# Kernel tuning notes

Hardware: AMD Instinct MI355X
Metric: run time of the kernel (lower is better)

Reference implementation:

```python
import jax, jax.numpy as jnp
import numpy as np

N = 131072   # octree nodes at this depth
C = 192      # channels (depthwise)
K = 27       # 3x3x3 neighbor stencil
BN_EPS = 1e-5


def setup_inputs() -> dict:
    key = jax.random.key(0)
    k1, k2, k3 = jax.random.split(key, 3)
    data = jax.random.normal(k1, (N, C), dtype=jnp.float32)
    # Octree neighbor table: for each node, indices of its 27 stencil neighbors.
    neigh = jax.random.randint(k2, (N, K), 0, N)
    # Depthwise weights [K, C] (OctreeDWConv, use_bias=False)
    weight = jax.random.normal(k3, (K, C), dtype=jnp.float32) * 0.05
    gamma = jnp.ones((C,), dtype=jnp.float32)
    beta = jnp.zeros((C,), dtype=jnp.float32)
    return {"data": data, "neigh": neigh, "weight": weight,
            "gamma": gamma, "beta": beta}


def reference(data, neigh, weight, gamma, beta):
    # Depthwise octree conv: out[n, c] = sum_k data[neigh[n, k], c] * weight[k, c]
    # Scan over the 27 stencil taps so we never materialize the [N, K, C] gather.
    def step(acc, kin):
        idx_k, w_k = kin          # idx_k: [N], w_k: [C]
        return acc + data[idx_k] * w_k, None

    acc0 = jnp.zeros_like(data)
    out, _ = jax.lax.scan(step, acc0, (neigh.T, weight))  # out: [N, C]

    # BatchNorm1d (training mode: batch statistics over the node dimension)
    mean = jnp.mean(out, axis=0)
    var = jnp.var(out, axis=0)
    return (out - mean) * jax.lax.rsqrt(var + BN_EPS) * gamma + beta
```

## Files before the change

### kernel.cpp

```cpp
#include <hip/hip_runtime.h>


static constexpr int NN = 131072;
static constexpr int CC = 192;
static constexpr int KK = 27;
static constexpr int NB = 32;
static constexpr float BN_EPS = 1e-5f;

__device__ __forceinline__ unsigned short f2bf_rne(float x) {
    unsigned u = __float_as_uint(x);
    return (unsigned short)((u + 0x7FFFu + ((u >> 16) & 1u)) >> 16);
}

__global__ __launch_bounds__(256) void cvt_zero(
    const float* __restrict__ src, unsigned short* __restrict__ dst,
    float* __restrict__ stats )
{
    if (blockIdx.x < 2 && threadIdx.x < CC)
        stats[blockIdx.x * CC + threadIdx.x] = 0.f;

    const int i = blockIdx.x * 256 + threadIdx.x;
    const float4 v = reinterpret_cast<const float4*>(src)[i];
    ushort4 o;
    o.x = f2bf_rne(v.x); o.y = f2bf_rne(v.y);
    o.z = f2bf_rne(v.z); o.w = f2bf_rne(v.w);
    reinterpret_cast<ushort4*>(dst)[i] = o;
}

__global__ __launch_bounds__(192, 8) void conv_r4(
    const unsigned short* __restrict__ data_bf,
    const int*   __restrict__ neigh,
    const float* __restrict__ weight,
    unsigned short* __restrict__ conv_bf,
    float*       __restrict__ ch_sum,
    float*       __restrict__ ch_sumsq)
{
    __shared__ float lds_w[KK * CC];

    const int c    = threadIdx.x;
    const int base = blockIdx.x * NB;

#pragma unroll
    for (int k = 0; k < KK; ++k) lds_w[k * CC + c] = weight[k * CC + c];
    __syncthreads();

    float s = 0.f, ss = 0.f;

    for (int n = 0; n < NB; ++n) {
        const int node = base + n;
        const int* nrow = neigh + node * KK;

        unsigned short r[KK];
#pragma unroll
        for (int k = 0; k < KK; ++k)
            r[k] = data_bf[(size_t)nrow[k] * CC + c];

        float acc = 0.f;
#pragma unroll
        for (int k = 0; k < KK; ++k)
            acc = fmaf(__uint_as_float((unsigned)r[k] << 16),
                       lds_w[k * CC + c], acc);

        conv_bf[(size_t)node * CC + c] = f2bf_rne(acc);
        s  += acc;
        ss += acc * acc;
    }

    atomicAdd(&ch_sum[c],   s);
    atomicAdd(&ch_sumsq[c], ss);
}

__global__ __launch_bounds__(192) void bn_apply_fused(
    const uint2* __restrict__ conv_bf,
    const float* __restrict__ ch_sum,
    const float* __restrict__ ch_sumsq,
    const float* __restrict__ gamma,
    const float* __restrict__ beta,
    float* __restrict__ out)
{
    const int t = threadIdx.x;
    const int g = t / 48;
    const int q = t - g * 48;
    const int cb = q * 4;

    const float inv_n = 1.0f / (float)NN;
    float4 sc, bi;
    {
        float m0 = ch_sum[cb + 0] * inv_n, m1 = ch_sum[cb + 1] * inv_n;
        float m2 = ch_sum[cb + 2] * inv_n, m3 = ch_sum[cb + 3] * inv_n;
        float v0 = ch_sumsq[cb + 0] * inv_n - m0 * m0;
        float v1 = ch_sumsq[cb + 1] * inv_n - m1 * m1;
        float v2 = ch_sumsq[cb + 2] * inv_n - m2 * m2;
        float v3 = ch_sumsq[cb + 3] * inv_n - m3 * m3;
        sc.x = gamma[cb + 0] * rsqrtf(v0 + BN_EPS);
        sc.y = gamma[cb + 1] * rsqrtf(v1 + BN_EPS);
        sc.z = gamma[cb + 2] * rsqrtf(v2 + BN_EPS);
        sc.w = gamma[cb + 3] * rsqrtf(v3 + BN_EPS);
        bi.x = beta[cb + 0] - m0 * sc.x;
        bi.y = beta[cb + 1] - m1 * sc.y;
        bi.z = beta[cb + 2] - m2 * sc.z;
        bi.w = beta[cb + 3] - m3 * sc.w;
    }

    for (int nb = blockIdx.x; nb < NN / 4; nb += gridDim.x) {
        const int node = nb * 4 + g;
        const int i = node * 48 + q;
        const uint2 u = conv_bf[i];
        float4 v;
        v.x = fmaf(__uint_as_float(u.x << 16),         sc.x, bi.x);
        v.y = fmaf(__uint_as_float(u.x & 0xFFFF0000u), sc.y, bi.y);
        v.z = fmaf(__uint_as_float(u.y << 16),         sc.z, bi.z);
        v.w = fmaf(__uint_as_float(u.y & 0xFFFF0000u), sc.w, bi.w);
        reinterpret_cast<float4*>(out)[i] = v;
    }
}

__global__ __launch_bounds__(CC) void conv_bn_partial_f32(
    const float* __restrict__ data,
    const int*   __restrict__ neigh,
    const float* __restrict__ weight,
    float*       __restrict__ conv_out,
    float*       __restrict__ ch_sum,
    float*       __restrict__ ch_sumsq)
{
    const int c = threadIdx.x;
    const int base = blockIdx.x * NB;
    if (blockIdx.x < 2 && c < CC) {  }
    float w[KK];
#pragma unroll
    for (int k = 0; k < KK; ++k) w[k] = weight[k * CC + c];
    float s = 0.f, ss = 0.f;
    for (int n = 0; n < NB; ++n) {
        const int node = base + n;
        const int* nrow = neigh + node * KK;
        float acc = 0.f;
#pragma unroll
        for (int k = 0; k < KK; ++k)
            acc = fmaf(data[nrow[k] * CC + c], w[k], acc);
        conv_out[node * CC + c] = acc;
        s += acc; ss += acc * acc;
    }
    atomicAdd(&ch_sum[c], s);
    atomicAdd(&ch_sumsq[c], ss);
}

__global__ __launch_bounds__(192) void bn_apply_f32_fused(
    float* __restrict__ out,
    const float* __restrict__ ch_sum,
    const float* __restrict__ ch_sumsq,
    const float* __restrict__ gamma,
    const float* __restrict__ beta)
{
    const int t = threadIdx.x;
    const int g = t / 48;
    const int q = t - g * 48;
    const int cb = q * 4;
    const float inv_n = 1.0f / (float)NN;
    float4 sc, bi;
    float m0 = ch_sum[cb+0]*inv_n, m1 = ch_sum[cb+1]*inv_n;
    float m2 = ch_sum[cb+2]*inv_n, m3 = ch_sum[cb+3]*inv_n;
    sc.x = gamma[cb+0]*rsqrtf(ch_sumsq[cb+0]*inv_n - m0*m0 + BN_EPS);
    sc.y = gamma[cb+1]*rsqrtf(ch_sumsq[cb+1]*inv_n - m1*m1 + BN_EPS);
    sc.z = gamma[cb+2]*rsqrtf(ch_sumsq[cb+2]*inv_n - m2*m2 + BN_EPS);
    sc.w = gamma[cb+3]*rsqrtf(ch_sumsq[cb+3]*inv_n - m3*m3 + BN_EPS);
    bi.x = beta[cb+0] - m0*sc.x; bi.y = beta[cb+1] - m1*sc.y;
    bi.z = beta[cb+2] - m2*sc.z; bi.w = beta[cb+3] - m3*sc.w;
    for (int nb = blockIdx.x; nb < NN / 4; nb += gridDim.x) {
        const int i = (nb * 4 + g) * 48 + q;
        float4 v = reinterpret_cast<float4*>(out)[i];
        v.x = fmaf(v.x, sc.x, bi.x); v.y = fmaf(v.y, sc.y, bi.y);
        v.z = fmaf(v.z, sc.z, bi.z); v.w = fmaf(v.w, sc.w, bi.w);
        reinterpret_cast<float4*>(out)[i] = v;
    }
}

extern "C" void kernel_launch(void* const* d_in, const int* in_sizes, int n_in,
                              void* d_out, int out_size, void* d_ws, size_t ws_size,
                              hipStream_t stream) {
    const float* data   = (const float*)d_in[0];
    const int*   neigh  = (const int*)  d_in[1];
    const float* weight = (const float*)d_in[2];
    const float* gamma  = (const float*)d_in[3];
    const float* beta   = (const float*)d_in[4];
    float* out = (float*)d_out;

    float* stats    = (float*)d_ws;
    float* ch_sum   = stats;
    float* ch_sumsq = stats + CC;
    unsigned short* data_bf = (unsigned short*)((char*)d_ws + 4096);
    const size_t stage_bytes = (size_t)NN * CC * sizeof(unsigned short);
    unsigned short* conv_bf =
        (unsigned short*)((char*)d_ws + 4096 + stage_bytes);

    const size_t need_full = 4096 + 2 * stage_bytes;
    const int vec_grid = (NN * CC / 4) / 256;

    if (ws_size >= need_full) {
        cvt_zero<<<vec_grid, 256, 0, stream>>>(data, data_bf, stats);
        conv_r4<<<NN / NB, 192, 0, stream>>>(
            data_bf, neigh, weight, conv_bf, ch_sum, ch_sumsq);
        bn_apply_fused<<<8192, 192, 0, stream>>>(
            (const uint2*)conv_bf, ch_sum, ch_sumsq, gamma, beta, out);
    } else {
        hipMemsetAsync(stats, 0, 2 * CC * sizeof(float), stream);
        conv_bn_partial_f32<<<NN / NB, CC, 0, stream>>>(
            data, neigh, weight, out, ch_sum, ch_sumsq);
        bn_apply_f32_fused<<<8192, 192, 0, stream>>>(
            out, ch_sum, ch_sumsq, gamma, beta);
    }
}
```

Measured before the change: 406.7 us.

## Fuse convert, conv and BN apply into one cooperative persistent kernel

Replaces the three launches (bf16 conversion with stats zeroing, gather conv with per-channel statistics, BN apply) with a single cooperative kernel. The grid is sized from the occupancy query, and the phases are separated by grid-wide syncs. The aim is to remove inter-kernel launch gaps and tail effects. In exchange it adds two grid barriers and a host occupancy query, and it turns the conv and apply phases into grid-stride loops over a smaller, persistent grid.

```diff
diff --git a/kernel.cpp b/kernel.cpp
--- a/kernel.cpp
+++ b/kernel.cpp
@@ -1,4 +1,7 @@
 #include <hip/hip_runtime.h>
+#include <hip/hip_cooperative_groups.h>
+
+namespace cg = cooperative_groups;
 
 
 static constexpr int NN = 131072;
@@ -12,106 +15,102 @@
     return (unsigned short)((u + 0x7FFFu + ((u >> 16) & 1u)) >> 16);
 }
 
-__global__ __launch_bounds__(256) void cvt_zero(
-    const float* __restrict__ src, unsigned short* __restrict__ dst,
-    float* __restrict__ stats )
-{
-    if (blockIdx.x < 2 && threadIdx.x < CC)
-        stats[blockIdx.x * CC + threadIdx.x] = 0.f;
-
-    const int i = blockIdx.x * 256 + threadIdx.x;
-    const float4 v = reinterpret_cast<const float4*>(src)[i];
-    ushort4 o;
-    o.x = f2bf_rne(v.x); o.y = f2bf_rne(v.y);
-    o.z = f2bf_rne(v.z); o.w = f2bf_rne(v.w);
-    reinterpret_cast<ushort4*>(dst)[i] = o;
-}
-
-__global__ __launch_bounds__(192, 8) void conv_r4(
-    const unsigned short* __restrict__ data_bf,
+__global__ __launch_bounds__(192, 8) void fused_all(
+    const float* __restrict__ data,
     const int*   __restrict__ neigh,
     const float* __restrict__ weight,
-    unsigned short* __restrict__ conv_bf,
-    float*       __restrict__ ch_sum,
-    float*       __restrict__ ch_sumsq)
-{
-    __shared__ float lds_w[KK * CC];
-
-    const int c    = threadIdx.x;
-    const int base = blockIdx.x * NB;
-
-#pragma unroll
-    for (int k = 0; k < KK; ++k) lds_w[k * CC + c] = weight[k * CC + c];
-    __syncthreads();
-
-    float s = 0.f, ss = 0.f;
-
-    for (int n = 0; n < NB; ++n) {
-        const int node = base + n;
-        const int* nrow = neigh + node * KK;
-
-        unsigned short r[KK];
-#pragma unroll
-        for (int k = 0; k < KK; ++k)
-            r[k] = data_bf[(size_t)nrow[k] * CC + c];
-
-        float acc = 0.f;
-#pragma unroll
-        for (int k = 0; k < KK; ++k)
-            acc = fmaf(__uint_as_float((unsigned)r[k] << 16),
-                       lds_w[k * CC + c], acc);
-
-        conv_bf[(size_t)node * CC + c] = f2bf_rne(acc);
-        s  += acc;
-        ss += acc * acc;
-    }
-
-    atomicAdd(&ch_sum[c],   s);
-    atomicAdd(&ch_sumsq[c], ss);
-}
-
-__global__ __launch_bounds__(192) void bn_apply_fused(
-    const uint2* __restrict__ conv_bf,
-    const float* __restrict__ ch_sum,
-    const float* __restrict__ ch_sumsq,
     const float* __restrict__ gamma,
     const float* __restrict__ beta,
+    unsigned short* __restrict__ data_bf,
+    unsigned short* __restrict__ conv_bf,
+    float* __restrict__ stats,
     float* __restrict__ out)
 {
+    cg::grid_group grid = cg::this_grid();
+    __shared__ float lds_w[KK * CC];
+
     const int t = threadIdx.x;
-    const int g = t / 48;
-    const int q = t - g * 48;
-    const int cb = q * 4;
-
-    const float inv_n = 1.0f / (float)NN;
-    float4 sc, bi;
+
+#pragma unroll
+    for (int k = 0; k < KK; ++k) lds_w[k * CC + t] = weight[k * CC + t];
+
+    if (blockIdx.x == 0) { stats[t] = 0.f; stats[CC + t] = 0.f; }
     {
-        float m0 = ch_sum[cb + 0] * inv_n, m1 = ch_sum[cb + 1] * inv_n;
-        float m2 = ch_sum[cb + 2] * inv_n, m3 = ch_sum[cb + 3] * inv_n;
-        float v0 = ch_sumsq[cb + 0] * inv_n - m0 * m0;
-        float v1 = ch_sumsq[cb + 1] * inv_n - m1 * m1;
-        float v2 = ch_sumsq[cb + 2] * inv_n - m2 * m2;
-        float v3 = ch_sumsq[cb + 3] * inv_n - m3 * m3;
-        sc.x = gamma[cb + 0] * rsqrtf(v0 + BN_EPS);
-        sc.y = gamma[cb + 1] * rsqrtf(v1 + BN_EPS);
-        sc.z = gamma[cb + 2] * rsqrtf(v2 + BN_EPS);
-        sc.w = gamma[cb + 3] * rsqrtf(v3 + BN_EPS);
-        bi.x = beta[cb + 0] - m0 * sc.x;
-        bi.y = beta[cb + 1] - m1 * sc.y;
-        bi.z = beta[cb + 2] - m2 * sc.z;
-        bi.w = beta[cb + 3] - m3 * sc.w;
-    }
-
-    for (int nb = blockIdx.x; nb < NN / 4; nb += gridDim.x) {
-        const int node = nb * 4 + g;
-        const int i = node * 48 + q;
-        const uint2 u = conv_bf[i];
-        float4 v;
-        v.x = fmaf(__uint_as_float(u.x << 16),         sc.x, bi.x);
-        v.y = fmaf(__uint_as_float(u.x & 0xFFFF0000u), sc.y, bi.y);
-        v.z = fmaf(__uint_as_float(u.y << 16),         sc.z, bi.z);
-        v.w = fmaf(__uint_as_float(u.y & 0xFFFF0000u), sc.w, bi.w);
-        reinterpret_cast<float4*>(out)[i] = v;
+        const int total4 = NN * CC / 4;
+        for (int i = blockIdx.x * 192 + t; i < total4; i += gridDim.x * 192) {
+            const float4 v = reinterpret_cast<const float4*>(data)[i];
+            ushort4 o;
+            o.x = f2bf_rne(v.x); o.y = f2bf_rne(v.y);
+            o.z = f2bf_rne(v.z); o.w = f2bf_rne(v.w);
+            reinterpret_cast<ushort4*>(data_bf)[i] = o;
+        }
+    }
+    grid.sync();
+
+    {
+        float s = 0.f, ss = 0.f;
+        for (int chunk = blockIdx.x; chunk < NN / NB; chunk += gridDim.x) {
+            const int base = chunk * NB;
+            for (int n = 0; n < NB; ++n) {
+                const int node = base + n;
+                const int* nrow = neigh + node * KK;
+
+                unsigned short r[KK];
+#pragma unroll
+                for (int k = 0; k < KK; ++k)
+                    r[k] = data_bf[(size_t)nrow[k] * CC + t];
+
+                float acc = 0.f;
+#pragma unroll
+                for (int k = 0; k < KK; ++k)
+                    acc = fmaf(__uint_as_float((unsigned)r[k] << 16),
+                               lds_w[k * CC + t], acc);
+
+                conv_bf[(size_t)node * CC + t] = f2bf_rne(acc);
+                s  += acc;
+                ss += acc * acc;
+            }
+        }
+        atomicAdd(&stats[t],      s);
+        atomicAdd(&stats[CC + t], ss);
+    }
+    grid.sync();
+
+    {
+        const int g  = t / 48;
+        const int q  = t - g * 48;
+        const int cb = q * 4;
+        const float inv_n = 1.0f / (float)NN;
+
+        float4 sc, bi;
+        {
+            const float m0 = stats[cb + 0] * inv_n, m1 = stats[cb + 1] * inv_n;
+            const float m2 = stats[cb + 2] * inv_n, m3 = stats[cb + 3] * inv_n;
+            const float v0 = stats[CC + cb + 0] * inv_n - m0 * m0;
+            const float v1 = stats[CC + cb + 1] * inv_n - m1 * m1;
+            const float v2 = stats[CC + cb + 2] * inv_n - m2 * m2;
+            const float v3 = stats[CC + cb + 3] * inv_n - m3 * m3;
+            sc.x = gamma[cb + 0] * rsqrtf(v0 + BN_EPS);
+            sc.y = gamma[cb + 1] * rsqrtf(v1 + BN_EPS);
+            sc.z = gamma[cb + 2] * rsqrtf(v2 + BN_EPS);
+            sc.w = gamma[cb + 3] * rsqrtf(v3 + BN_EPS);
+            bi.x = beta[cb + 0] - m0 * sc.x;
+            bi.y = beta[cb + 1] - m1 * sc.y;
+            bi.z = beta[cb + 2] - m2 * sc.z;
+            bi.w = beta[cb + 3] - m3 * sc.w;
+        }
+
+        const uint2* cbf = reinterpret_cast<const uint2*>(conv_bf);
+        for (int nb = blockIdx.x; nb < NN / 4; nb += gridDim.x) {
+            const int i = (nb * 4 + g) * 48 + q;
+            const uint2 u = cbf[i];
+            float4 v;
+            v.x = fmaf(__uint_as_float(u.x << 16),         sc.x, bi.x);
+            v.y = fmaf(__uint_as_float(u.x & 0xFFFF0000u), sc.y, bi.y);
+            v.z = fmaf(__uint_as_float(u.y << 16),         sc.z, bi.z);
+            v.w = fmaf(__uint_as_float(u.y & 0xFFFF0000u), sc.w, bi.w);
+            reinterpret_cast<float4*>(out)[i] = v;
+        }
     }
 }
 
@@ -125,7 +124,6 @@
 {
     const int c = threadIdx.x;
     const int base = blockIdx.x * NB;
-    if (blockIdx.x < 2 && c < CC) {  }
     float w[KK];
 #pragma unroll
     for (int k = 0; k < KK; ++k) w[k] = weight[k * CC + c];
@@ -157,8 +155,8 @@
     const int cb = q * 4;
     const float inv_n = 1.0f / (float)NN;
     float4 sc, bi;
-    float m0 = ch_sum[cb+0]*inv_n, m1 = ch_sum[cb+1]*inv_n;
-    float m2 = ch_sum[cb+2]*inv_n, m3 = ch_sum[cb+3]*inv_n;
+    const float m0 = ch_sum[cb+0]*inv_n, m1 = ch_sum[cb+1]*inv_n;
+    const float m2 = ch_sum[cb+2]*inv_n, m3 = ch_sum[cb+3]*inv_n;
     sc.x = gamma[cb+0]*rsqrtf(ch_sumsq[cb+0]*inv_n - m0*m0 + BN_EPS);
     sc.y = gamma[cb+1]*rsqrtf(ch_sumsq[cb+1]*inv_n - m1*m1 + BN_EPS);
     sc.z = gamma[cb+2]*rsqrtf(ch_sumsq[cb+2]*inv_n - m2*m2 + BN_EPS);
@@ -184,28 +182,41 @@
     const float* beta   = (const float*)d_in[4];
     float* out = (float*)d_out;
 
-    float* stats    = (float*)d_ws;
-    float* ch_sum   = stats;
-    float* ch_sumsq = stats + CC;
+    float* stats = (float*)d_ws;
     unsigned short* data_bf = (unsigned short*)((char*)d_ws + 4096);
     const size_t stage_bytes = (size_t)NN * CC * sizeof(unsigned short);
     unsigned short* conv_bf =
         (unsigned short*)((char*)d_ws + 4096 + stage_bytes);
-
     const size_t need_full = 4096 + 2 * stage_bytes;
-    const int vec_grid = (NN * CC / 4) / 256;
-
-    if (ws_size >= need_full) {
-        cvt_zero<<<vec_grid, 256, 0, stream>>>(data, data_bf, stats);
-        conv_r4<<<NN / NB, 192, 0, stream>>>(
-            data_bf, neigh, weight, conv_bf, ch_sum, ch_sumsq);
-        bn_apply_fused<<<8192, 192, 0, stream>>>(
-            (const uint2*)conv_bf, ch_sum, ch_sumsq, gamma, beta, out);
-    } else {
-        hipMemsetAsync(stats, 0, 2 * CC * sizeof(float), stream);
-        conv_bn_partial_f32<<<NN / NB, CC, 0, stream>>>(
-            data, neigh, weight, out, ch_sum, ch_sumsq);
-        bn_apply_f32_fused<<<8192, 192, 0, stream>>>(
-            out, ch_sum, ch_sumsq, gamma, beta);
-    }
-}
+
+    bool coop_ok = (ws_size >= need_full);
+    int grid_blocks = 0;
+    if (coop_ok) {
+        int blocks_per_cu = 0;
+        hipError_t e = hipOccupancyMaxActiveBlocksPerMultiprocessor(
+            &blocks_per_cu, (const void*)fused_all, 192, 0);
+        if (e != hipSuccess || blocks_per_cu < 1) coop_ok = false;
+        else grid_blocks = blocks_per_cu * 256;
+        if (grid_blocks > NN / NB) grid_blocks = NN / NB;
+    }
+
+    if (coop_ok) {
+        void* args[] = {
+            (void*)&data, (void*)&neigh, (void*)&weight,
+            (void*)&gamma, (void*)&beta,
+            (void*)&data_bf, (void*)&conv_bf, (void*)&stats, (void*)&out
+        };
+        hipError_t e = hipLaunchCooperativeKernel(
+            (const void*)fused_all, dim3(grid_blocks), dim3(192),
+            args, 0, stream);
+        if (e == hipSuccess) return;
+    }
+
+    float* ch_sum   = stats;
+    float* ch_sumsq = stats + CC;
+    hipMemsetAsync(stats, 0, 2 * CC * sizeof(float), stream);
+    conv_bn_partial_f32<<<NN / NB, CC, 0, stream>>>(
+        data, neigh, weight, out, ch_sum, ch_sumsq);
+    bn_apply_f32_fused<<<8192, 192, 0, stream>>>(
+        out, ch_sum, ch_sumsq, gamma, beta);
+}
```

Result: slower. 611.8 us (+50.4%).
